# Kernel optimization log

Hardware: AMD Instinct MI355X
Metric: run time of the kernel (lower is better)

## Reference

```python
import jax, jax.numpy as jnp
import numpy as np

B, N, FIN = 32, 1024, 6
KCHEB = 3
CLASS_NUM = 40


def _pairwise_adj(x):
    # x: [B, N, D] -> exp(-squared_euclidean_dist) adjacency [B, N, N]
    inner = jnp.einsum('bnd,bmd->bnm', x, x)
    sq = jnp.sum(x * x, axis=-1)
    d2 = sq[:, :, None] - 2.0 * inner + sq[:, None, :]
    return jnp.exp(-d2)


def _get_laplacian(adj):
    # normalized Laplacian: I - D^{-1/2} A D^{-1/2}
    deg = jnp.sum(adj, axis=-1)                       # [B, N]
    d_is = 1.0 / jnp.sqrt(deg)                        # [B, N]
    eye = jnp.eye(adj.shape[-1], dtype=adj.dtype)
    return eye - d_is[:, :, None] * adj * d_is[:, None, :]


def _cheb_conv(x, L, W, b):
    # Chebyshev graph conv: sum_k T_k(L) x W_k + b;  W: [K, Fin, Fout]
    x0 = x
    x1 = jnp.einsum('bnm,bmf->bnf', L, x0)
    out = jnp.einsum('bnf,fg->bng', x0, W[0]) + jnp.einsum('bnf,fg->bng', x1, W[1])
    xk_2, xk_1 = x0, x1
    for k in range(2, W.shape[0]):
        xk = 2.0 * jnp.einsum('bnm,bmf->bnf', L, xk_1) - xk_2
        out = out + jnp.einsum('bnf,fg->bng', xk, W[k])
        xk_2, xk_1 = xk_1, xk
    return out + b


def setup_inputs() -> dict:
    key = jax.random.key(0)
    ks = jax.random.split(key, 16)

    def w(k, shape, fan_in):
        return jax.random.normal(k, shape, dtype=jnp.float32) / np.sqrt(fan_in)

    return {
        'x': jax.random.normal(ks[0], (B, N, FIN), dtype=jnp.float32),
        'W1': w(ks[1], (KCHEB, 6, 128), 6 * KCHEB),
        'b1': jnp.zeros((128,), jnp.float32),
        'W2': w(ks[2], (KCHEB, 128, 512), 128 * KCHEB),
        'b2': jnp.zeros((512,), jnp.float32),
        'W3': w(ks[3], (KCHEB, 512, 1024), 512 * KCHEB),
        'b3': jnp.zeros((1024,), jnp.float32),
        'fc1_w': w(ks[4], (1024, 512), 1024),
        'fc1_b': jnp.zeros((512,), jnp.float32),
        'fc2_w': w(ks[5], (512, 128), 512),
        'fc2_b': jnp.zeros((128,), jnp.float32),
        'fc3_w': w(ks[6], (128, CLASS_NUM), 128),
        'fc3_b': jnp.zeros((CLASS_NUM,), jnp.float32),
    }


def reference(x, W1, b1, W2, b2, W3, b3, fc1_w, fc1_b, fc2_w, fc2_b, fc3_w, fc3_b):
    # Laplacians are computed under torch.no_grad in the original
    L = _get_laplacian(_pairwise_adj(x))
    out = jax.nn.relu(_cheb_conv(x, L, W1, b1))        # [B, N, 128]

    L = _get_laplacian(_pairwise_adj(out))
    out = jax.nn.relu(_cheb_conv(out, L, W2, b2))      # [B, N, 512]

    L = _get_laplacian(_pairwise_adj(out))
    out = jax.nn.relu(_cheb_conv(out, L, W3, b3))      # [B, N, 1024]

    out = jnp.max(out, axis=1)                          # global max pool -> [B, 1024]
    out = jax.nn.relu(out @ fc1_w + fc1_b)              # dropout is identity at eval
    out = jax.nn.relu(out @ fc2_w + fc2_b)
    out = out @ fc3_w + fc3_b                           # [B, CLASS_NUM]
    return out
```

## Files before the change

kernel.cpp:

```cpp
#include <hip/hip_runtime.h>
#include <cstddef>


#define NN 1024

typedef unsigned short ushort_t;
typedef __bf16 bf16x8 __attribute__((ext_vector_type(8)));
typedef float f32x4 __attribute__((ext_vector_type(4)));

__device__ inline ushort_t f2bf(float f) {
    unsigned int u = __float_as_uint(f);
    u = (u + 0x7fffu + ((u >> 16) & 1u)) >> 16;
    return (ushort_t)u;
}
__device__ inline float bf2f(ushort_t s) {
    return __uint_as_float(((unsigned int)s) << 16);
}

__device__ __attribute__((always_inline)) inline void gld16(
    const ushort_t* g, ushort_t* l) {
    __builtin_amdgcn_global_load_lds(
        (__attribute__((address_space(1))) void*)(ushort_t*)g,
        (__attribute__((address_space(3))) void*)l, 16, 0, 0);
}

__global__ __launch_bounds__(256) void init_kernel(
    const float* __restrict__ W1, const float* __restrict__ W2,
    const float* __restrict__ W3, ushort_t* __restrict__ Wt,
    float* __restrict__ pool) {
    __shared__ float T[64][65];
    int bid = blockIdx.x, t = threadIdx.x;
    if (bid < 16) {
#pragma unroll
        for (int k = 0; k < 8; ++k) pool[bid * 2048 + k * 256 + t] = 0.f;
        return;
    }
    bid -= 16;
    const float* W; ushort_t* wt; int Fi, Fo, Ks, gx, gy, p;
    if (bid < 6)       { W = W1; wt = Wt;          Fi = 6;   Fo = 128;  Ks = 32;
                         gx = bid % 2; gy = 0; p = bid / 2; }
    else if (bid < 54) { int b = bid - 6;  W = W2; wt = Wt + 12288;  Fi = 128; Fo = 512;  Ks = 128;
                         gx = b % 8; gy = (b / 8) % 2; p = b / 16; }
    else               { int b = bid - 54; W = W3; wt = Wt + 208896; Fi = 512; Fo = 1024; Ks = 512;
                         gx = b % 16; gy = (b / 16) % 8; p = b / 128; }
    int k0 = gy * 64, g0 = gx * 64;
#pragma unroll
    for (int q = 0; q < 16; ++q) {
        int kr = (t >> 6) + 4 * q, gc = t & 63;
        int k = k0 + kr, g = g0 + gc;
        T[kr][gc] = (k < Fi && g < Fo) ? W[((size_t)p * Fi + k) * Fo + g] : 0.f;
    }
    __syncthreads();
#pragma unroll
    for (int q = 0; q < 16; ++q) {
        int gr = (t >> 6) + 4 * q, kc = t & 63;
        int g = g0 + gr, k = k0 + kc;
        if (g < Fo && k < Ks)
            wt[((size_t)p * Fo + g) * Ks + k] = f2bf(T[kc][gr]);
    }
}

__global__ __launch_bounds__(256) void prep2_kernel(
    const float* __restrict__ X, ushort_t* __restrict__ hi, ushort_t* __restrict__ lo,
    ushort_t* __restrict__ Xt, float* __restrict__ sq, int F, int Fp, int bsh) {
    int L = blockIdx.x;
    int b = L & ((1 << bsh) - 1), n0 = (L >> bsh) * 64;
    int t = threadIdx.x;
    __shared__ float T[64][65];
    __shared__ float red[4][64];
    const float* Xb = X ? (X + ((size_t)b * NN + n0) * F) : nullptr;
    const ushort_t* hb = hi + ((size_t)b * NN + n0) * Fp;
    const ushort_t* lb = lo + ((size_t)b * NN + n0) * Fp;
    float sacc = 0.f;

    for (int f0 = 0; f0 < Fp; f0 += 64) {
        __syncthreads();
#pragma unroll
        for (int p = 0; p < 16; ++p) {
            int nr = (t >> 6) + 4 * p, fc = t & 63;
            int f = f0 + fc;
            float xv = 0.f;
            if (f < F) {
                if (Xb) xv = Xb[(size_t)nr * F + f];
                else {
                    size_t off = (size_t)nr * Fp + f;
                    xv = bf2f(hb[off]) + bf2f(lb[off]);
                }
            }
            T[nr][fc] = xv;
        }
        __syncthreads();
        if (Xb) {
#pragma unroll
            for (int p = 0; p < 16; ++p) {
                int nr = (t >> 6) + 4 * p, fc = t & 63;
                int f = f0 + fc;
                if (f < Fp) {
                    float x = T[nr][fc];
                    ushort_t h = f2bf(x);
                    size_t off = ((size_t)b * NN + n0 + nr) * Fp + f;
                    hi[off] = h;
                    lo[off] = f2bf(x - bf2f(h));
                }
            }
        }
#pragma unroll
        for (int p = 0; p < 16; ++p) {
            int fr = (t >> 6) + 4 * p;
            int f = f0 + fr;
            if (f < F)
                Xt[((size_t)b * Fp + f) * NN + n0 + (t & 63)] = f2bf(T[t & 63][fr]);
        }
        {
            int nl = t & 63, fq = t >> 6;
#pragma unroll
            for (int fc = 0; fc < 16; ++fc) {
                float v = T[nl][fq * 16 + fc];
                sacc += v * v;
            }
        }
    }
    red[t >> 6][t & 63] = sacc;
    __syncthreads();
    if (t < 64)
        sq[(size_t)b * NN + n0 + t] = red[0][t] + red[1][t] + red[2][t] + red[3][t];
}

__global__ __launch_bounds__(256) void adj_kernel(
    const ushort_t* __restrict__ hi, const ushort_t* __restrict__ lo,
    const float* __restrict__ sq, ushort_t* __restrict__ Abf,
    float* __restrict__ deg_part, int Fp, int bsh, int BCv) {
    int t = threadIdx.x;
    int L = blockIdx.x;
    int b = L & ((1 << bsh) - 1);
    int rest = L >> bsh;
    int ti = 0;
    while (rest >= 8 - ti) { rest -= 8 - ti; ++ti; }
    int tj = ti + rest;
    int n0 = ti * 128, m0 = tj * 128;
    const ushort_t* Hb = hi + (size_t)b * NN * Fp;
    const ushort_t* Lb = lo + (size_t)b * NN * Fp;
    ushort_t* Ab = Abf + (size_t)b * NN * NN;
    const float* sqb = sq + (size_t)b * NN;

    int lane = t & 63, quad = lane >> 4, l16 = lane & 15, wave = t >> 6;
    int rowoff = (wave >> 1) * 64, coloff = (wave & 1) * 64;

    __shared__ __align__(16) ushort_t smem[40960];

    f32x4 acc[4][4];
#pragma unroll
    for (int i = 0; i < 4; ++i)
#pragma unroll
        for (int j = 0; j < 4; ++j) acc[i][j] = (f32x4){0.f, 0.f, 0.f, 0.f};

    int rr0 = t >> 2, kq = (t & 3) * 8;
    int rr1 = rr0 + 64;
    const ushort_t* pAh0 = Hb + (size_t)(n0 + rr0) * Fp + kq;
    const ushort_t* pAh1 = Hb + (size_t)(n0 + rr1) * Fp + kq;
    const ushort_t* pAl0 = Lb + (size_t)(n0 + rr0) * Fp + kq;
    const ushort_t* pAl1 = Lb + (size_t)(n0 + rr1) * Fp + kq;
    const ushort_t* pBh0 = Hb + (size_t)(m0 + rr0) * Fp + kq;
    const ushort_t* pBh1 = Hb + (size_t)(m0 + rr1) * Fp + kq;
    const ushort_t* pBl0 = Lb + (size_t)(m0 + rr0) * Fp + kq;
    const ushort_t* pBl1 = Lb + (size_t)(m0 + rr1) * Fp + kq;
    int o0 = rr0 * 40 + kq, o1 = rr1 * 40 + kq;

    {
        *(uint4*)&smem[o0]         = *(const uint4*)pAh0;
        *(uint4*)&smem[o1]         = *(const uint4*)pAh1;
        *(uint4*)&smem[5120 + o0]  = *(const uint4*)pAl0;
        *(uint4*)&smem[5120 + o1]  = *(const uint4*)pAl1;
        *(uint4*)&smem[10240 + o0] = *(const uint4*)pBh0;
        *(uint4*)&smem[10240 + o1] = *(const uint4*)pBh1;
        *(uint4*)&smem[15360 + o0] = *(const uint4*)pBl0;
        *(uint4*)&smem[15360 + o1] = *(const uint4*)pBl1;
    }
    __syncthreads();

    int NIT = Fp >> 5;
    for (int it = 0; it < NIT; ++it) {
        int cur = (it & 1) * 20480;
        int nxt = 20480 - cur;
        uint4 rh0, rh1, rl0, rl1, sh0, sh1, sl0, sl1;
        if (it + 1 < NIT) {
            int k = (it + 1) * 32;
            rh0 = *(const uint4*)(pAh0 + k); rh1 = *(const uint4*)(pAh1 + k);
            rl0 = *(const uint4*)(pAl0 + k); rl1 = *(const uint4*)(pAl1 + k);
            sh0 = *(const uint4*)(pBh0 + k); sh1 = *(const uint4*)(pBh1 + k);
            sl0 = *(const uint4*)(pBl0 + k); sl1 = *(const uint4*)(pBl1 + k);
        }
        ushort_t* Ah = smem + cur;
        ushort_t* Al = smem + cur + 5120;
        ushort_t* Bh = smem + cur + 10240;
        ushort_t* Bl = smem + cur + 15360;
        bf16x8 ah[4], al[4], bh[4], bl[4];
#pragma unroll
        for (int i = 0; i < 4; ++i) {
            ah[i] = *(const bf16x8*)&Ah[(rowoff + i * 16 + l16) * 40 + quad * 8];
            al[i] = *(const bf16x8*)&Al[(rowoff + i * 16 + l16) * 40 + quad * 8];
        }
#pragma unroll
        for (int j = 0; j < 4; ++j) {
            bh[j] = *(const bf16x8*)&Bh[(coloff + j * 16 + l16) * 40 + quad * 8];
            bl[j] = *(const bf16x8*)&Bl[(coloff + j * 16 + l16) * 40 + quad * 8];
        }
#pragma unroll
        for (int i = 0; i < 4; ++i)
#pragma unroll
            for (int j = 0; j < 4; ++j) {
                acc[i][j] = __builtin_amdgcn_mfma_f32_16x16x32_bf16(al[i], bh[j], acc[i][j], 0, 0, 0);
                acc[i][j] = __builtin_amdgcn_mfma_f32_16x16x32_bf16(ah[i], bl[j], acc[i][j], 0, 0, 0);
                acc[i][j] = __builtin_amdgcn_mfma_f32_16x16x32_bf16(ah[i], bh[j], acc[i][j], 0, 0, 0);
            }
        if (it + 1 < NIT) {
            *(uint4*)&smem[nxt + o0]         = rh0;
            *(uint4*)&smem[nxt + o1]         = rh1;
            *(uint4*)&smem[nxt + 5120 + o0]  = rl0;
            *(uint4*)&smem[nxt + 5120 + o1]  = rl1;
            *(uint4*)&smem[nxt + 10240 + o0] = sh0;
            *(uint4*)&smem[nxt + 10240 + o1] = sh1;
            *(uint4*)&smem[nxt + 15360 + o0] = sl0;
            *(uint4*)&smem[nxt + 15360 + o1] = sl1;
        }
        __syncthreads();
    }

    bool offdiag = (ti != tj);
    float rs[4][4];
    float cs[4] = {0.f, 0.f, 0.f, 0.f};
#pragma unroll
    for (int i = 0; i < 4; ++i)
#pragma unroll
        for (int r = 0; r < 4; ++r) rs[i][r] = 0.f;

#pragma unroll
    for (int j = 0; j < 4; ++j) {
        int ml = coloff + j * 16 + l16;
        float sm = sqb[m0 + ml];
#pragma unroll
        for (int i = 0; i < 4; ++i) {
#pragma unroll
            for (int r = 0; r < 4; ++r) {
                int nl = rowoff + i * 16 + quad * 4 + r;
                float v = __expf(2.f * acc[i][j][r] - sqb[n0 + nl] - sm);
                rs[i][r] += v;
                ushort_t vb = f2bf(v);
                smem[nl * 128 + (((ml >> 3) ^ (nl & 7)) << 3) + (ml & 7)] = vb;
                if (offdiag) {
                    cs[j] += v;
                    smem[16384 + ml * 128 + (((nl >> 3) ^ (ml & 7)) << 3) + (nl & 7)] = vb;
                }
            }
        }
    }
    __syncthreads();
    for (int s2 = t; s2 < 2048; s2 += 256) {
        int nl = s2 >> 4, oct = s2 & 15;
        uint4 v4 = *(const uint4*)&smem[nl * 128 + ((oct ^ (nl & 7)) << 3)];
        *(uint4*)(Ab + (size_t)(n0 + nl) * NN + m0 + oct * 8) = v4;
    }

    int slot = tj * 2 + (wave & 1);
#pragma unroll
    for (int i = 0; i < 4; ++i)
#pragma unroll
        for (int r = 0; r < 4; ++r) {
            float s = rs[i][r];
            s += __shfl_xor(s, 1);
            s += __shfl_xor(s, 2);
            s += __shfl_xor(s, 4);
            s += __shfl_xor(s, 8);
            if (l16 == 0)
                deg_part[((size_t)slot * BCv + b) * NN + n0 + rowoff + i * 16 + quad * 4 + r] = s;
        }

    if (offdiag) {
#pragma unroll
        for (int j = 0; j < 4; ++j) {
            float s = cs[j];
            s += __shfl_xor(s, 16);
            s += __shfl_xor(s, 32);
            cs[j] = s;
        }
        if (quad == 0) {
#pragma unroll
            for (int j = 0; j < 4; ++j)
                deg_part[((size_t)(ti * 2 + (wave >> 1)) * BCv + b) * NN +
                         m0 + coloff + j * 16 + l16] = cs[j];
        }
        for (int s2 = t; s2 < 2048; s2 += 256) {
            int ml = s2 >> 4, oct = s2 & 15;
            uint4 v4 = *(const uint4*)&smem[16384 + ml * 128 + ((oct ^ (ml & 7)) << 3)];
            *(uint4*)(Ab + (size_t)(m0 + ml) * NN + n0 + oct * 8) = v4;
        }
    }
}

__global__ __launch_bounds__(256) void disscale_kernel(
    ushort_t* __restrict__ Xt, const float* __restrict__ deg_part,
    float* __restrict__ dis, int Fp, int bsh, int BCv) {
    int L = blockIdx.x;
    int b = L & ((1 << bsh) - 1), n0 = (L >> bsh) * 64;
    int t = threadIdx.x;
    __shared__ float dloc[64];
    if (t < 64) {
        float s = 0.f;
#pragma unroll
        for (int k = 0; k < 16; ++k) s += deg_part[((size_t)k * BCv + b) * NN + n0 + t];
        float d = rsqrtf(s);
        dloc[t] = d;
        dis[(size_t)b * NN + n0 + t] = d;
    }
    __syncthreads();
    int lane = t & 63, fq = t >> 6;
    float d = dloc[lane];
    ushort_t* Xb = Xt + (size_t)b * Fp * NN + n0 + lane;
    for (int f = fq; f < Fp; f += 4) {
        size_t off = (size_t)f * NN;
        Xb[off] = f2bf(bf2f(Xb[off]) * d);
    }
}

__global__ __launch_bounds__(256) void lx_kernel(
    const ushort_t* __restrict__ Abf, const float* __restrict__ dis,
    const ushort_t* __restrict__ in_t, const ushort_t* __restrict__ x0t,
    ushort_t* __restrict__ out_t, ushort_t* __restrict__ out_b,
    int F, int Fp, int mode, int ft, int bsh) {
    int t = threadIdx.x;
    int L = blockIdx.x;
    int b = L & ((1 << bsh) - 1);
    int rest = L >> bsh;
    int m0 = (rest % ft) * 128;
    int n0 = (rest / ft) * 64;
    const ushort_t* Ain = in_t + (size_t)b * Fp * NN;
    const ushort_t* Ab = Abf + (size_t)b * NN * NN;

    int lane = t & 63, quad = lane >> 4, l16 = lane & 15, wave = t >> 6;
    int rowoff = wave * 32;

    __shared__ __align__(16) ushort_t smem[18432];

    f32x4 acc[2][4];
#pragma unroll
    for (int i = 0; i < 2; ++i)
#pragma unroll
        for (int j = 0; j < 4; ++j) acc[i][j] = (f32x4){0.f, 0.f, 0.f, 0.f};

    int lr = lane >> 2, lk = (lane & 3) * 8;
    int rbase = wave * 32;
    const ushort_t* gA = Ain + (size_t)(m0 + rbase + lr) * NN + lk;
    const ushort_t* gB = Ab + (size_t)(n0 + wave * 16 + lr) * NN + lk;

#define LX_STAGE(BOFF, CI)                                            \
    {                                                                 \
        int k_ = (CI) * 32;                                           \
        ushort_t* As_ = smem + (BOFF);                                \
        gld16(gA + k_, As_ + rbase * 32);                             \
        gld16(gA + (size_t)16 * NN + k_, As_ + rbase * 32 + 512);     \
        gld16(gB + k_, As_ + 4096 + wave * 16 * 32);                  \
    }
#define LX_COMP(BOFF)                                                            \
    {                                                                            \
        ushort_t* As_ = smem + (BOFF);                                           \
        ushort_t* Bs_ = As_ + 4096;                                              \
        bf16x8 af[2], bfv[4];                                                    \
        _Pragma("unroll")                                                        \
        for (int i = 0; i < 2; ++i)                                              \
            af[i] = *(const bf16x8*)&As_[(rowoff + i * 16 + l16) * 32 + quad * 8]; \
        _Pragma("unroll")                                                        \
        for (int j = 0; j < 4; ++j)                                              \
            bfv[j] = *(const bf16x8*)&Bs_[(j * 16 + l16) * 32 + quad * 8];       \
        _Pragma("unroll")                                                        \
        for (int i = 0; i < 2; ++i)                                              \
            _Pragma("unroll")                                                    \
            for (int j = 0; j < 4; ++j)                                          \
                acc[i][j] = __builtin_amdgcn_mfma_f32_16x16x32_bf16(af[i], bfv[j], acc[i][j], 0, 0, 0); \
    }

    LX_STAGE(0, 0);
    LX_STAGE(6144, 1);
    int cur = 0;
    for (int ci = 0; ci < 32; ++ci) {
        if (ci < 31) { asm volatile("s_waitcnt vmcnt(3)" ::: "memory"); }
        else         { asm volatile("s_waitcnt vmcnt(0)" ::: "memory"); }
        __builtin_amdgcn_s_barrier();
        asm volatile("" ::: "memory");
        if (ci + 2 < 32) {
            int noff = cur + 12288; if (noff >= 18432) noff -= 18432;
            LX_STAGE(noff, ci + 2);
        }
        LX_COMP(cur);
        cur += 6144; if (cur >= 18432) cur = 0;
    }
#undef LX_STAGE
#undef LX_COMP
    __syncthreads();

#pragma unroll
    for (int j = 0; j < 4; ++j) {
        int nl = j * 16 + l16;
        int n = n0 + nl;
        float dn = dis[(size_t)b * NN + n];
        float inv = 1.f / dn;
        float dn2 = dn * dn;
#pragma unroll
        for (int i = 0; i < 2; ++i) {
#pragma unroll
            for (int r = 0; r < 4; ++r) {
                int fl = rowoff + i * 16 + quad * 4 + r;
                int f = m0 + fl;
                float o = 0.f;
                if (f < F) {
                    float a = acc[i][j][r];
                    size_t off = (size_t)f * NN + n;
                    float xin = bf2f(Ain[off]);
                    if (mode == 0) {
                        out_t[(size_t)b * Fp * NN + off] = f2bf(xin - dn2 * a);
                        o = inv * xin - dn * a;
                    } else {
                        float x0 = bf2f(x0t[(size_t)b * Fp * NN + off]);
                        o = inv * (2.f * xin - x0) - 2.f * dn * a;
                    }
                }
                smem[nl * 128 + (((fl >> 3) ^ (nl & 7)) << 3) + (fl & 7)] = f2bf(o);
            }
        }
    }
    __syncthreads();
    for (int s2 = t; s2 < 1024; s2 += 256) {
        int nl = s2 >> 4, oct = s2 & 15;
        int fg = m0 + oct * 8;
        if (fg < Fp) {
            uint4 v = *(const uint4*)&smem[nl * 128 + ((oct ^ (nl & 7)) << 3)];
            *(uint4*)(out_b + ((size_t)b * NN + n0 + nl) * Fp + fg) = v;
        }
    }
}

__global__ __launch_bounds__(512) void proj_kernel(
    const ushort_t* __restrict__ X0, const ushort_t* __restrict__ X1,
    const ushort_t* __restrict__ X2, const ushort_t* __restrict__ Wt,
    const float* __restrict__ bias, ushort_t* __restrict__ Ohi,
    ushort_t* __restrict__ Olo, float* __restrict__ pool,
    int Fp, int Fo, int b0, int n_g, int bsh) {
    int t = threadIdx.x;
    int L = blockIdx.x;
    int c = L & ((1 << bsh) - 1);
    int rest = L >> bsh;
    int g0 = (rest % n_g) * 128;
    int r0 = (c * 4 + rest / n_g) * 256;
    int lane = t & 63, quad = lane >> 4, l16 = lane & 15, wave = t >> 6;
    int rowoff = (wave >> 1) * 64, coloff = (wave & 1) * 64;

    __shared__ __align__(16) ushort_t smem[36864];

    f32x4 acc[4][4];
#pragma unroll
    for (int i = 0; i < 4; ++i)
#pragma unroll
        for (int j = 0; j < 4; ++j) acc[i][j] = (f32x4){0.f, 0.f, 0.f, 0.f};

    int lr = lane >> 2, lk = (lane & 3) * 8;
    int nk = Fp >> 5;
    int NIT = 3 * nk;
    size_t FoFp = (size_t)Fo * Fp;
    size_t r16 = (size_t)16 * Fp;

#define PJ_STAGE(BOFF, CI)                                                    \
    {                                                                         \
        int p_ = (CI) / nk;                                                   \
        int k_ = ((CI) - p_ * nk) * 32 + lk;                                  \
        const ushort_t* Xp_ = (p_ == 0) ? X0 : ((p_ == 1) ? X1 : X2);         \
        const ushort_t* ga_ = Xp_ + (size_t)(r0 + wave * 32 + lr) * Fp + k_;  \
        const ushort_t* gb_ = Wt + (size_t)p_ * FoFp +                        \
                              (size_t)(g0 + wave * 16 + lr) * Fp + k_;        \
        ushort_t* As_ = smem + (BOFF) + wave * 1024;                          \
        ushort_t* Bs_ = smem + (BOFF) + 8192 + wave * 512;                    \
        gld16(ga_, As_);                                                      \
        gld16(ga_ + r16, As_ + 512);                                          \
        gld16(gb_, Bs_);                                                      \
    }
#define PJ_COMP(BOFF)                                                           \
    {                                                                           \
        ushort_t* As_ = smem + (BOFF);                                          \
        ushort_t* Bs_ = As_ + 8192;                                             \
        bf16x8 af[4], bfv[4];                                                   \
        _Pragma("unroll")                                                       \
        for (int i = 0; i < 4; ++i)                                             \
            af[i] = *(const bf16x8*)&As_[(rowoff + i * 16 + l16) * 32 + quad * 8];  \
        _Pragma("unroll")                                                       \
        for (int j = 0; j < 4; ++j)                                             \
            bfv[j] = *(const bf16x8*)&Bs_[(coloff + j * 16 + l16) * 32 + quad * 8]; \
        _Pragma("unroll")                                                       \
        for (int i = 0; i < 4; ++i)                                             \
            _Pragma("unroll")                                                   \
            for (int j = 0; j < 4; ++j)                                         \
                acc[i][j] = __builtin_amdgcn_mfma_f32_16x16x32_bf16(af[i], bfv[j], acc[i][j], 0, 0, 0); \
    }

    PJ_STAGE(0, 0);
    PJ_STAGE(12288, 1);
    int cur = 0;
    for (int ci = 0; ci < NIT; ++ci) {
        if (ci < NIT - 1) { asm volatile("s_waitcnt vmcnt(3)" ::: "memory"); }
        else              { asm volatile("s_waitcnt vmcnt(0)" ::: "memory"); }
        __builtin_amdgcn_s_barrier();
        asm volatile("" ::: "memory");
        if (ci + 2 < NIT) {
            int noff = cur + 24576; if (noff >= 36864) noff -= 36864;
            PJ_STAGE(noff, ci + 2);
        }
        PJ_COMP(cur);
        cur += 12288; if (cur >= 36864) cur = 0;
    }
#undef PJ_STAGE
#undef PJ_COMP

    float bias_l[4];
#pragma unroll
    for (int j = 0; j < 4; ++j) bias_l[j] = bias[g0 + coloff + j * 16 + l16];

    if (Ohi) {
#pragma unroll
        for (int i = 0; i < 4; ++i) {
#pragma unroll
            for (int r = 0; r < 4; ++r) {
                int row = r0 + rowoff + i * 16 + quad * 4 + r;
#pragma unroll
                for (int j = 0; j < 4; ++j) {
                    int g = g0 + coloff + j * 16 + l16;
                    float o = fmaxf(acc[i][j][r] + bias_l[j], 0.f);
                    ushort_t h = f2bf(o);
                    size_t off = (size_t)row * Fo + g;
                    Ohi[off] = h;
                    Olo[off] = f2bf(o - bf2f(h));
                }
            }
        }
    } else {
        float mj[4];
#pragma unroll
        for (int j = 0; j < 4; ++j) {
            float m = 0.f;
#pragma unroll
            for (int i = 0; i < 4; ++i)
#pragma unroll
                for (int r = 0; r < 4; ++r)
                    m = fmaxf(m, acc[i][j][r] + bias_l[j]);
            m = fmaxf(m, 0.f);
            m = fmaxf(m, __shfl_xor(m, 16));
            m = fmaxf(m, __shfl_xor(m, 32));
            mj[j] = m;
        }
        if (quad == 0) {
            int smp = b0 + (r0 >> 10);
#pragma unroll
            for (int j = 0; j < 4; ++j)
                atomicMax((int*)&pool[(size_t)smp * 1024 + g0 + coloff + j * 16 + l16],
                          __float_as_int(mj[j]));
        }
    }
}

__global__ __launch_bounds__(256) void fc_kernel(
    const float* __restrict__ In, const float* __restrict__ W,
    const float* __restrict__ bias, float* __restrict__ out,
    int K, int Nout, int relu) {
    int r = blockIdx.y;
    int c0 = blockIdx.x * 64;
    int t = threadIdx.x;
    int cl = t & 63, ks = t >> 6;
    int c = c0 + cl;
    int kchunk = K >> 2;
    int k0 = ks * kchunk, k1 = k0 + kchunk;
    float s = 0.f;
    if (c < Nout) {
        const float* ip = In + (size_t)r * K;
        const float* wp = W + c;
#pragma unroll 4
        for (int k = k0; k < k1; ++k) s += ip[k] * wp[(size_t)k * Nout];
    }
    __shared__ float red[4][64];
    red[ks][cl] = s;
    __syncthreads();
    if (t < 64 && c0 + t < Nout) {
        float v = red[0][t] + red[1][t] + red[2][t] + red[3][t] + bias[c0 + t];
        if (relu) v = fmaxf(v, 0.f);
        out[(size_t)r * Nout + c0 + t] = v;
    }
}

extern "C" void kernel_launch(void* const* d_in, const int* in_sizes, int n_in,
                              void* d_out, int out_size, void* d_ws, size_t ws_size,
                              hipStream_t stream) {
    const float* x    = (const float*)d_in[0];
    const float* W1   = (const float*)d_in[1];
    const float* b1   = (const float*)d_in[2];
    const float* W2   = (const float*)d_in[3];
    const float* b2   = (const float*)d_in[4];
    const float* W3   = (const float*)d_in[5];
    const float* b3   = (const float*)d_in[6];
    const float* fc1w = (const float*)d_in[7];
    const float* fc1b = (const float*)d_in[8];
    const float* fc2w = (const float*)d_in[9];
    const float* fc2b = (const float*)d_in[10];
    const float* fc3w = (const float*)d_in[11];
    const float* fc3b = (const float*)d_in[12];
    float* out = (float*)d_out;

    auto need = [](size_t BCv) -> size_t {
        size_t us = (size_t)BCv * 1024;
        return 2 * (us * 1024) + 10 * (us * 512) + 2 * 1781760ull +
               4 * us + 64 * us + 4 * us +
               4 * (32768ull + 16384 + 4096) + 256;
    };
    int BCv = (ws_size >= need(32)) ? 32 : (ws_size >= need(16)) ? 16 : 8;
    int NCH = 32 / BCv;
    int bsh = (BCv == 32) ? 5 : (BCv == 16) ? 4 : 3;

    size_t usc = (size_t)BCv * 1024;
    size_t Asz = usc * 1024;
    size_t SLv = usc * 512;
    ushort_t* Abf = (ushort_t*)d_ws;
    ushort_t* S[5];
    S[0] = Abf + Asz;
    for (int i = 1; i < 5; ++i) S[i] = S[i - 1] + SLv;
    ushort_t* Wt = S[4] + SLv;
    float* sq   = (float*)(Wt + 1781760);
    float* degp = sq + usc;
    float* dis  = degp + 16 * usc;
    float* pool = dis + usc;
    float* f1   = pool + 32768;
    float* f2   = f1 + 16384;

    init_kernel<<<454, 256, 0, stream>>>(W1, W2, W3, Wt, pool);

    const int MP[3][5] = {{0, 1, 2, 3, 4}, {3, 2, 0, 4, 1}, {4, 0, 3, 1, 2}};

    for (int c = 0; c < NCH; ++c) {
        int b0 = c * BCv;
        struct LayerDef {
            int F, Fp, Fo;
            const ushort_t* Wtl; const float* bias;
        };
        LayerDef L[3] = {
            { 6,   32,  128,  Wt,          b1 },
            { 128, 128, 512,  Wt + 12288,  b2 },
            { 512, 512, 1024, Wt + 208896, b3 },
        };
        for (int li = 0; li < 3; ++li) {
            LayerDef& Ld = L[li];
            int F = Ld.F, Fp = Ld.Fp;
            int ft = (F + 127) / 128;
            int n_g = Ld.Fo / 128;
            ushort_t* xhi = S[MP[li][0]];
            ushort_t* xlo = S[MP[li][1]];
            ushort_t* Xt  = S[MP[li][2]];
            ushort_t* X1t = S[MP[li][3]];
            ushort_t* X1b = S[MP[li][4]];
            prep2_kernel<<<16 * BCv, 256, 0, stream>>>(
                (li == 0) ? (x + (size_t)b0 * NN * 6) : nullptr,
                xhi, xlo, Xt, sq, F, Fp, bsh);
            adj_kernel<<<36 * BCv, 256, 0, stream>>>(xhi, xlo, sq, Abf, degp, Fp, bsh, BCv);
            disscale_kernel<<<16 * BCv, 256, 0, stream>>>(Xt, degp, dis, Fp, bsh, BCv);
            lx_kernel<<<ft * 16 * BCv, 256, 0, stream>>>(
                Abf, dis, Xt, nullptr, X1t, X1b, F, Fp, 0, ft, bsh);
            lx_kernel<<<ft * 16 * BCv, 256, 0, stream>>>(
                Abf, dis, X1t, Xt, nullptr, xlo, F, Fp, 1, ft, bsh);
            proj_kernel<<<n_g * 4 * BCv, 512, 0, stream>>>(
                xhi, X1b, xlo, Ld.Wtl, Ld.bias,
                (li < 2) ? X1t : nullptr, (li < 2) ? Xt : nullptr,
                pool, Fp, Ld.Fo, b0, n_g, bsh);
        }
    }

    fc_kernel<<<dim3(8, 32), 256, 0, stream>>>(pool, fc1w, fc1b, f1, 1024, 512, 1);
    fc_kernel<<<dim3(2, 32), 256, 0, stream>>>(f1, fc2w, fc2b, f2, 512, 128, 1);
    fc_kernel<<<dim3(1, 32), 256, 0, stream>>>(f2, fc3w, fc3b, out, 128, 40, 0);
}
```

Measured before the change: 798.7 us.

## Enlarge L·X tile to 128x128 per block and fuse FC head kernels

The lx_kernel output tile grows from 128x64 to 128x128, with four waves in a 2x2 layout each computing a 64x64 sub-tile. Each wave now also loads half of the B (adjacency) tile, so every staged A tile is reused across twice as many columns and the grid halves. The three FC launches are merged into one kernel per sample that keeps the intermediates in shared memory. The cost is more accumulator registers and more LDS per block, which may lower occupancy, and the fused FC layer runs on only 32 blocks.

```diff
diff --git a/kernel.cpp b/kernel.cpp
--- a/kernel.cpp
+++ b/kernel.cpp
@@ -332,66 +332,67 @@
     int b = L & ((1 << bsh) - 1);
     int rest = L >> bsh;
     int m0 = (rest % ft) * 128;
-    int n0 = (rest / ft) * 64;
+    int n0 = (rest / ft) * 128;
     const ushort_t* Ain = in_t + (size_t)b * Fp * NN;
     const ushort_t* Ab = Abf + (size_t)b * NN * NN;
 
     int lane = t & 63, quad = lane >> 4, l16 = lane & 15, wave = t >> 6;
-    int rowoff = wave * 32;
-
-    __shared__ __align__(16) ushort_t smem[18432];
-
-    f32x4 acc[2][4];
-#pragma unroll
-    for (int i = 0; i < 2; ++i)
+    int rowoff = (wave >> 1) * 64, coloff = (wave & 1) * 64;
+
+    __shared__ __align__(16) ushort_t smem[24576];
+
+    f32x4 acc[4][4];
+#pragma unroll
+    for (int i = 0; i < 4; ++i)
 #pragma unroll
         for (int j = 0; j < 4; ++j) acc[i][j] = (f32x4){0.f, 0.f, 0.f, 0.f};
 
     int lr = lane >> 2, lk = (lane & 3) * 8;
-    int rbase = wave * 32;
-    const ushort_t* gA = Ain + (size_t)(m0 + rbase + lr) * NN + lk;
-    const ushort_t* gB = Ab + (size_t)(n0 + wave * 16 + lr) * NN + lk;
+    const ushort_t* gA = Ain + (size_t)(m0 + wave * 32 + lr) * NN + lk;
+    const ushort_t* gB = Ab + (size_t)(n0 + wave * 32 + lr) * NN + lk;
 
 #define LX_STAGE(BOFF, CI)                                            \
     {                                                                 \
         int k_ = (CI) * 32;                                           \
-        ushort_t* As_ = smem + (BOFF);                                \
-        gld16(gA + k_, As_ + rbase * 32);                             \
-        gld16(gA + (size_t)16 * NN + k_, As_ + rbase * 32 + 512);     \
-        gld16(gB + k_, As_ + 4096 + wave * 16 * 32);                  \
+        ushort_t* As_ = smem + (BOFF) + wave * 1024;                  \
+        ushort_t* Bs_ = smem + (BOFF) + 4096 + wave * 1024;           \
+        gld16(gA + k_, As_);                                          \
+        gld16(gA + (size_t)16 * NN + k_, As_ + 512);                  \
+        gld16(gB + k_, Bs_);                                          \
+        gld16(gB + (size_t)16 * NN + k_, Bs_ + 512);                  \
     }
 #define LX_COMP(BOFF)                                                            \
     {                                                                            \
         ushort_t* As_ = smem + (BOFF);                                           \
         ushort_t* Bs_ = As_ + 4096;                                              \
-        bf16x8 af[2], bfv[4];                                                    \
+        bf16x8 af[4], bfv[4];                                                    \
         _Pragma("unroll")                                                        \
-        for (int i = 0; i < 2; ++i)                                              \
+        for (int i = 0; i < 4; ++i)                                              \
             af[i] = *(const bf16x8*)&As_[(rowoff + i * 16 + l16) * 32 + quad * 8]; \
         _Pragma("unroll")                                                        \
         for (int j = 0; j < 4; ++j)                                              \
-            bfv[j] = *(const bf16x8*)&Bs_[(j * 16 + l16) * 32 + quad * 8];       \
+            bfv[j] = *(const bf16x8*)&Bs_[(coloff + j * 16 + l16) * 32 + quad * 8]; \
         _Pragma("unroll")                                                        \
-        for (int i = 0; i < 2; ++i)                                              \
+        for (int i = 0; i < 4; ++i)                                              \
             _Pragma("unroll")                                                    \
             for (int j = 0; j < 4; ++j)                                          \
                 acc[i][j] = __builtin_amdgcn_mfma_f32_16x16x32_bf16(af[i], bfv[j], acc[i][j], 0, 0, 0); \
     }
 
     LX_STAGE(0, 0);
-    LX_STAGE(6144, 1);
+    LX_STAGE(8192, 1);
     int cur = 0;
     for (int ci = 0; ci < 32; ++ci) {
-        if (ci < 31) { asm volatile("s_waitcnt vmcnt(3)" ::: "memory"); }
+        if (ci < 31) { asm volatile("s_waitcnt vmcnt(4)" ::: "memory"); }
         else         { asm volatile("s_waitcnt vmcnt(0)" ::: "memory"); }
         __builtin_amdgcn_s_barrier();
         asm volatile("" ::: "memory");
         if (ci + 2 < 32) {
-            int noff = cur + 12288; if (noff >= 18432) noff -= 18432;
+            int noff = cur + 16384; if (noff >= 24576) noff -= 24576;
             LX_STAGE(noff, ci + 2);
         }
         LX_COMP(cur);
-        cur += 6144; if (cur >= 18432) cur = 0;
+        cur += 8192; if (cur >= 24576) cur = 0;
     }
 #undef LX_STAGE
 #undef LX_COMP
@@ -399,13 +400,13 @@
 
 #pragma unroll
     for (int j = 0; j < 4; ++j) {
-        int nl = j * 16 + l16;
+        int nl = coloff + j * 16 + l16;
         int n = n0 + nl;
         float dn = dis[(size_t)b * NN + n];
         float inv = 1.f / dn;
         float dn2 = dn * dn;
 #pragma unroll
-        for (int i = 0; i < 2; ++i) {
+        for (int i = 0; i < 4; ++i) {
 #pragma unroll
             for (int r = 0; r < 4; ++r) {
                 int fl = rowoff + i * 16 + quad * 4 + r;
@@ -428,7 +429,7 @@
         }
     }
     __syncthreads();
-    for (int s2 = t; s2 < 1024; s2 += 256) {
+    for (int s2 = t; s2 < 2048; s2 += 256) {
         int nl = s2 >> 4, oct = s2 & 15;
         int fg = m0 + oct * 8;
         if (fg < Fp) {
@@ -563,31 +564,42 @@
     }
 }
 
-__global__ __launch_bounds__(256) void fc_kernel(
-    const float* __restrict__ In, const float* __restrict__ W,
-    const float* __restrict__ bias, float* __restrict__ out,
-    int K, int Nout, int relu) {
-    int r = blockIdx.y;
-    int c0 = blockIdx.x * 64;
-    int t = threadIdx.x;
-    int cl = t & 63, ks = t >> 6;
-    int c = c0 + cl;
-    int kchunk = K >> 2;
-    int k0 = ks * kchunk, k1 = k0 + kchunk;
-    float s = 0.f;
-    if (c < Nout) {
-        const float* ip = In + (size_t)r * K;
-        const float* wp = W + c;
+__global__ __launch_bounds__(256) void fc_fused_kernel(
+    const float* __restrict__ In, const float* __restrict__ w1,
+    const float* __restrict__ bb1, const float* __restrict__ w2,
+    const float* __restrict__ bb2, const float* __restrict__ w3,
+    const float* __restrict__ bb3, float* __restrict__ out) {
+    int r = blockIdx.x, t = threadIdx.x;
+    __shared__ float p[1024];
+    __shared__ float f1s[512];
+    __shared__ float f2s[128];
+#pragma unroll
+    for (int k = 0; k < 4; ++k) p[k * 256 + t] = In[(size_t)r * 1024 + k * 256 + t];
+    __syncthreads();
+#pragma unroll
+    for (int cc = 0; cc < 2; ++cc) {
+        int c = cc * 256 + t;
+        float s = 0.f;
+        const float* wp = w1 + c;
 #pragma unroll 4
-        for (int k = k0; k < k1; ++k) s += ip[k] * wp[(size_t)k * Nout];
-    }
-    __shared__ float red[4][64];
-    red[ks][cl] = s;
-    __syncthreads();
-    if (t < 64 && c0 + t < Nout) {
-        float v = red[0][t] + red[1][t] + red[2][t] + red[3][t] + bias[c0 + t];
-        if (relu) v = fmaxf(v, 0.f);
-        out[(size_t)r * Nout + c0 + t] = v;
+        for (int k = 0; k < 1024; ++k) s += p[k] * wp[(size_t)k * 512];
+        f1s[c] = fmaxf(s + bb1[c], 0.f);
+    }
+    __syncthreads();
+    if (t < 128) {
+        float s = 0.f;
+        const float* wp = w2 + t;
+#pragma unroll 4
+        for (int k = 0; k < 512; ++k) s += f1s[k] * wp[(size_t)k * 128];
+        f2s[t] = fmaxf(s + bb2[t], 0.f);
+    }
+    __syncthreads();
+    if (t < 40) {
+        float s = 0.f;
+        const float* wp = w3 + t;
+#pragma unroll 4
+        for (int k = 0; k < 128; ++k) s += f2s[k] * wp[(size_t)k * 40];
+        out[(size_t)r * 40 + t] = s + bb3[t];
     }
 }
 
@@ -633,6 +645,7 @@
     float* pool = dis + usc;
     float* f1   = pool + 32768;
     float* f2   = f1 + 16384;
+    (void)f1; (void)f2;
 
     init_kernel<<<454, 256, 0, stream>>>(W1, W2, W3, Wt, pool);
 
@@ -664,9 +677,9 @@
                 xhi, xlo, Xt, sq, F, Fp, bsh);
             adj_kernel<<<36 * BCv, 256, 0, stream>>>(xhi, xlo, sq, Abf, degp, Fp, bsh, BCv);
             disscale_kernel<<<16 * BCv, 256, 0, stream>>>(Xt, degp, dis, Fp, bsh, BCv);
-            lx_kernel<<<ft * 16 * BCv, 256, 0, stream>>>(
+            lx_kernel<<<ft * 8 * BCv, 256, 0, stream>>>(
                 Abf, dis, Xt, nullptr, X1t, X1b, F, Fp, 0, ft, bsh);
-            lx_kernel<<<ft * 16 * BCv, 256, 0, stream>>>(
+            lx_kernel<<<ft * 8 * BCv, 256, 0, stream>>>(
                 Abf, dis, X1t, Xt, nullptr, xlo, F, Fp, 1, ft, bsh);
             proj_kernel<<<n_g * 4 * BCv, 512, 0, stream>>>(
                 xhi, X1b, xlo, Ld.Wtl, Ld.bias,
@@ -675,7 +688,6 @@
         }
     }
 
-    fc_kernel<<<dim3(8, 32), 256, 0, stream>>>(pool, fc1w, fc1b, f1, 1024, 512, 1);
-    fc_kernel<<<dim3(2, 32), 256, 0, stream>>>(f1, fc2w, fc2b, f2, 512, 128, 1);
-    fc_kernel<<<dim3(1, 32), 256, 0, stream>>>(f2, fc3w, fc3b, out, 128, 40, 0);
-}
+    fc_fused_kernel<<<32, 256, 0, stream>>>(pool, fc1w, fc1b, fc2w, fc2b,
+                                            fc3w, fc3b, out);
+}
```

After: 1.051 ms. 1.32x slower.
